# Kernel tuning notes

Measured on AMD Instinct MI355X. Metric: run time of the kernel, lower is better.

The kernel has to match this reference:

```python
import jax, jax.numpy as jnp
import numpy as np

M, B, T, D, P = 3, 128, 512, 1024, 256  # modalities, batch, time, d_model, projection_dim
LN_EPS = 1e-5
NORM_EPS = 1e-12


def setup_inputs() -> dict:
    key = jax.random.key(0)
    ks = jax.random.split(key, 7)
    s1 = 1.0 / np.sqrt(D)
    s2 = 1.0 / np.sqrt(D)
    return {
        "feats": jax.random.normal(ks[0], (M, B, T, D), dtype=jnp.float32),
        "W1": jax.random.uniform(ks[1], (M, D, D), jnp.float32, -s1, s1),
        "b1": jax.random.uniform(ks[2], (M, D), jnp.float32, -s1, s1),
        "W2": jax.random.uniform(ks[3], (M, D, P), jnp.float32, -s2, s2),
        "b2": jax.random.uniform(ks[4], (M, P), jnp.float32, -s2, s2),
        "gamma": jnp.ones((M, P), jnp.float32),
        "beta": jnp.zeros((M, P), jnp.float32),
    }


def reference(feats, W1, b1, W2, b2, gamma, beta):
    # Mean-pool over time: [M,B,T,D] -> [M,B,D]
    pooled = feats.mean(axis=2)
    # Linear(d_model, d_model) + exact GELU (dropout is identity at inference)
    h = jax.nn.gelu(jnp.einsum('mbd,mde->mbe', pooled, W1) + b1[:, None, :],
                    approximate=False)
    # Linear(d_model, projection_dim)
    z = jnp.einsum('mbd,mdp->mbp', h, W2) + b2[:, None, :]
    # LayerNorm over last dim
    mu = z.mean(axis=-1, keepdims=True)
    var = jnp.mean((z - mu) ** 2, axis=-1, keepdims=True)
    z = (z - mu) / jnp.sqrt(var + LN_EPS) * gamma[:, None, :] + beta[:, None, :]
    # F.normalize (cosine path): divide by max(l2_norm, eps)
    n = jnp.sqrt(jnp.sum(z * z, axis=-1, keepdims=True))
    return z / jnp.maximum(n, NORM_EPS)  # [M, B, P]
```

## Files before the change

kernel.cpp:

```cpp
#include <hip/hip_runtime.h>
#include <math.h>

#define M_ 3
#define B_ 128
#define T_ 512
#define D_ 1024
#define P_ 256
#define TC 4
#define BM1 32
#define BN1 64
#define BK1 64
#define LDA1 (BK1 + 4)
#define G  2

__global__ __launch_bounds__(256) void pool_partial(const float* __restrict__ feats,
                                                    float* __restrict__ partial) {
    int blk = blockIdx.x;
    int tc  = blk & (TC - 1);
    int mb  = blk / TC;
    int tid = threadIdx.x;
    const int TSTEP = T_ / TC;
    const float4* src = (const float4*)feats + ((size_t)mb * T_ + (size_t)tc * TSTEP) * (D_ / 4) + tid;
    float4 a0 = make_float4(0.f, 0.f, 0.f, 0.f);
    float4 a1 = a0, a2 = a0, a3 = a0;
    for (int t = 0; t < TSTEP; t += 4) {
        float4 v0 = src[0 * (D_ / 4)];
        float4 v1 = src[1 * (D_ / 4)];
        float4 v2 = src[2 * (D_ / 4)];
        float4 v3 = src[3 * (D_ / 4)];
        src += 4 * (D_ / 4);
        a0.x += v0.x; a0.y += v0.y; a0.z += v0.z; a0.w += v0.w;
        a1.x += v1.x; a1.y += v1.y; a1.z += v1.z; a1.w += v1.w;
        a2.x += v2.x; a2.y += v2.y; a2.z += v2.z; a2.w += v2.w;
        a3.x += v3.x; a3.y += v3.y; a3.z += v3.z; a3.w += v3.w;
    }
    float4 s;
    s.x = (a0.x + a1.x) + (a2.x + a3.x);
    s.y = (a0.y + a1.y) + (a2.y + a3.y);
    s.z = (a0.z + a1.z) + (a2.z + a3.z);
    s.w = (a0.w + a1.w) + (a2.w + a3.w);
    ((float4*)partial)[((size_t)mb * TC + tc) * (D_ / 4) + tid] = s;
}

__global__ __launch_bounds__(256) void pool_finalize(const float* __restrict__ partial,
                                                     float* __restrict__ pooled) {
    int idx = blockIdx.x * 256 + threadIdx.x;
    int mb  = idx >> 8;
    int d4  = idx & 255;
    const float4* p4 = (const float4*)partial;
    float4 s = make_float4(0.f, 0.f, 0.f, 0.f);
#pragma unroll
    for (int tc = 0; tc < TC; ++tc) {
        float4 v = p4[((size_t)mb * TC + tc) * (D_ / 4) + d4];
        s.x += v.x; s.y += v.y; s.z += v.z; s.w += v.w;
    }
    const float inv = 1.0f / (float)T_;
    s.x *= inv; s.y *= inv; s.z *= inv; s.w *= inv;
    ((float4*)pooled)[idx] = s;
}

__global__ __launch_bounds__(256) void gemm1_gelu(const float* __restrict__ pooled,
                                                  const float* __restrict__ W1,
                                                  const float* __restrict__ b1,
                                                  float* __restrict__ h) {
    __shared__ float As[BM1][LDA1];
    __shared__ float Bs[BK1][BN1];
    int m  = blockIdx.z;
    int b0 = blockIdx.y * BM1;
    int e0 = blockIdx.x * BN1;
    int tid = threadIdx.x;
    int ar  = tid >> 4;
    int ac4 = tid & 15;
    int ty  = tid >> 4;
    int tx  = tid & 15;

    const float* Abase = pooled + ((size_t)m * B_ + b0) * D_;
    const float* Bbase = W1 + (size_t)m * D_ * D_ + e0;

    float4 acc0 = make_float4(0.f, 0.f, 0.f, 0.f);
    float4 acc1 = make_float4(0.f, 0.f, 0.f, 0.f);

    for (int k0 = 0; k0 < D_; k0 += BK1) {
        float4 av0 = *(const float4*)(Abase + (size_t)ar * D_ + k0 + ac4 * 4);
        float4 av1 = *(const float4*)(Abase + (size_t)(ar + 16) * D_ + k0 + ac4 * 4);
        float4 bv0 = *(const float4*)(Bbase + (size_t)(k0 + ar) * D_ + ac4 * 4);
        float4 bv1 = *(const float4*)(Bbase + (size_t)(k0 + ar + 16) * D_ + ac4 * 4);
        float4 bv2 = *(const float4*)(Bbase + (size_t)(k0 + ar + 32) * D_ + ac4 * 4);
        float4 bv3 = *(const float4*)(Bbase + (size_t)(k0 + ar + 48) * D_ + ac4 * 4);
        __syncthreads();
        *(float4*)&As[ar][ac4 * 4]      = av0;
        *(float4*)&As[ar + 16][ac4 * 4] = av1;
        *(float4*)&Bs[ar][ac4 * 4]      = bv0;
        *(float4*)&Bs[ar + 16][ac4 * 4] = bv1;
        *(float4*)&Bs[ar + 32][ac4 * 4] = bv2;
        *(float4*)&Bs[ar + 48][ac4 * 4] = bv3;
        __syncthreads();
#pragma unroll
        for (int k = 0; k < BK1; ++k) {
            float a0 = As[2 * ty][k];
            float a1 = As[2 * ty + 1][k];
            float4 b = *(float4*)&Bs[k][tx * 4];
            acc0.x += a0 * b.x; acc0.y += a0 * b.y; acc0.z += a0 * b.z; acc0.w += a0 * b.w;
            acc1.x += a1 * b.x; acc1.y += a1 * b.y; acc1.z += a1 * b.z; acc1.w += a1 * b.w;
        }
    }
    int col = e0 + tx * 4;
    float4 bb = *(const float4*)(b1 + m * D_ + col);
    float4 z0, z1;
    z0.x = acc0.x + bb.x; z0.y = acc0.y + bb.y; z0.z = acc0.z + bb.z; z0.w = acc0.w + bb.w;
    z1.x = acc1.x + bb.x; z1.y = acc1.y + bb.y; z1.z = acc1.z + bb.z; z1.w = acc1.w + bb.w;
    const float is2 = 0.70710678118654752f;
    float4 g0, g1;
    g0.x = 0.5f * z0.x * (1.0f + erff(z0.x * is2));
    g0.y = 0.5f * z0.y * (1.0f + erff(z0.y * is2));
    g0.z = 0.5f * z0.z * (1.0f + erff(z0.z * is2));
    g0.w = 0.5f * z0.w * (1.0f + erff(z0.w * is2));
    g1.x = 0.5f * z1.x * (1.0f + erff(z1.x * is2));
    g1.y = 0.5f * z1.y * (1.0f + erff(z1.y * is2));
    g1.z = 0.5f * z1.z * (1.0f + erff(z1.z * is2));
    g1.w = 0.5f * z1.w * (1.0f + erff(z1.w * is2));
    int row0 = b0 + 2 * ty;
    *(float4*)&h[((size_t)m * B_ + row0) * D_ + col]     = g0;
    *(float4*)&h[((size_t)m * B_ + row0 + 1) * D_ + col] = g1;
}

__global__ __launch_bounds__(256) void gemm2_ln(const float* __restrict__ h,
                                                const float* __restrict__ W2,
                                                const float* __restrict__ b2,
                                                const float* __restrict__ gamma,
                                                const float* __restrict__ beta,
                                                float* __restrict__ out) {
    int m  = blockIdx.y;
    int b0 = blockIdx.x * G;
    int tid = threadIdx.x;
    int lane = tid & 63, w = tid >> 6;

    __shared__ float red1[4][G];
    __shared__ float red2[4][G];

    const float* W2base = W2 + (size_t)m * D_ * P_ + tid;
    const float* hbase  = h + ((size_t)m * B_ + b0) * D_;

    float acc[G];
#pragma unroll
    for (int g = 0; g < G; ++g) acc[g] = 0.f;

#pragma unroll 4
    for (int k4 = 0; k4 < D_ / 4; ++k4) {
        float w0 = W2base[(size_t)(4 * k4 + 0) * P_];
        float w1 = W2base[(size_t)(4 * k4 + 1) * P_];
        float w2 = W2base[(size_t)(4 * k4 + 2) * P_];
        float w3 = W2base[(size_t)(4 * k4 + 3) * P_];
#pragma unroll
        for (int g = 0; g < G; ++g) {
            float4 hv = *(const float4*)(hbase + (size_t)g * D_ + 4 * k4);
            acc[g] += hv.x * w0 + hv.y * w1 + hv.z * w2 + hv.w * w3;
        }
    }

    float bias = b2[m * P_ + tid];
    float gm   = gamma[m * P_ + tid];
    float bt   = beta[m * P_ + tid];

    float z[G];
#pragma unroll
    for (int g = 0; g < G; ++g) z[g] = acc[g] + bias;

#pragma unroll
    for (int g = 0; g < G; ++g) {
        float s1 = z[g], s2 = z[g] * z[g];
        for (int off = 32; off > 0; off >>= 1) {
            s1 += __shfl_xor(s1, off);
            s2 += __shfl_xor(s2, off);
        }
        if (lane == 0) { red1[w][g] = s1; red2[w][g] = s2; }
    }
    __syncthreads();
#pragma unroll
    for (int g = 0; g < G; ++g) {
        float s1 = (red1[0][g] + red1[1][g]) + (red1[2][g] + red1[3][g]);
        float s2 = (red2[0][g] + red2[1][g]) + (red2[2][g] + red2[3][g]);
        float mu  = s1 * (1.0f / P_);
        float var = s2 * (1.0f / P_) - mu * mu;
        float inv = 1.0f / sqrtf(var + 1e-5f);
        z[g] = (z[g] - mu) * inv * gm + bt;
    }
    __syncthreads();

#pragma unroll
    for (int g = 0; g < G; ++g) {
        float s = z[g] * z[g];
        for (int off = 32; off > 0; off >>= 1) s += __shfl_xor(s, off);
        if (lane == 0) red1[w][g] = s;
    }
    __syncthreads();
#pragma unroll
    for (int g = 0; g < G; ++g) {
        float s = (red1[0][g] + red1[1][g]) + (red1[2][g] + red1[3][g]);
        float n = sqrtf(s);
        out[((size_t)m * B_ + b0 + g) * P_ + tid] = z[g] / fmaxf(n, 1e-12f);
    }
}

extern "C" void kernel_launch(void* const* d_in, const int* in_sizes, int n_in,
                              void* d_out, int out_size, void* d_ws, size_t ws_size,
                              hipStream_t stream) {
    const float* feats = (const float*)d_in[0];
    const float* W1    = (const float*)d_in[1];
    const float* b1    = (const float*)d_in[2];
    const float* W2    = (const float*)d_in[3];
    const float* b2    = (const float*)d_in[4];
    const float* gamma = (const float*)d_in[5];
    const float* beta  = (const float*)d_in[6];
    float* out = (float*)d_out;

    float* wsf     = (float*)d_ws;
    float* partial = wsf;
    float* pooled  = wsf + (size_t)M_ * B_ * TC * D_;
    float* hbuf    = pooled + (size_t)M_ * B_ * D_;

    pool_partial<<<M_ * B_ * TC, 256, 0, stream>>>(feats, partial);
    pool_finalize<<<(M_ * B_ * D_ / 4) / 256, 256, 0, stream>>>(partial, pooled);
    dim3 g3(D_ / BN1, B_ / BM1, M_);
    gemm1_gelu<<<g3, 256, 0, stream>>>(pooled, W1, b1, hbuf);
    dim3 g4(B_ / G, M_);
    gemm2_ln<<<g4, 256, 0, stream>>>(hbuf, W2, b2, gamma, beta, out);
}
```

Before: 219.6 us.

## Fuse pool finalize into GEMM1, split-K both GEMMs, cast W2 to bf16

Removes the pool_finalize kernel by having GEMM1 sum the TC=2 partial sums and scale by 1/T while loading A. Pooling now uses two time chunks per row with eight accumulators instead of four. Both GEMMs run 512 threads with an intra-block split-K whose halves are combined through shared memory. Extra blocks in the pooling launch convert W2 to packed bf16 so GEMM2 reads half the weight bytes, at the cost of reduced precision in the second projection.

```diff
diff --git a/kernel.cpp b/kernel.cpp
--- a/kernel.cpp
+++ b/kernel.cpp
@@ -6,200 +6,221 @@
 #define T_ 512
 #define D_ 1024
 #define P_ 256
-#define TC 4
+#define TC 2
+#define NRIDER 64
 #define BM1 32
 #define BN1 64
-#define BK1 64
-#define LDA1 (BK1 + 4)
-#define G  2
-
-__global__ __launch_bounds__(256) void pool_partial(const float* __restrict__ feats,
-                                                    float* __restrict__ partial) {
+
+__device__ __forceinline__ unsigned int f2bf(float f) {
+    unsigned int x = __float_as_uint(f);
+    return (x + 0x7fffu + ((x >> 16) & 1u)) >> 16;
+}
+
+__global__ __launch_bounds__(256) void pool_and_cast(const float* __restrict__ feats,
+                                                     const float* __restrict__ W2,
+                                                     float* __restrict__ partial,
+                                                     unsigned int* __restrict__ w2p) {
     int blk = blockIdx.x;
-    int tc  = blk & (TC - 1);
-    int mb  = blk / TC;
     int tid = threadIdx.x;
+    if (blk < NRIDER) {
+        const int TOT = M_ * (D_ / 2) * P_;
+        for (int i = blk * 256 + tid; i < TOT; i += NRIDER * 256) {
+            int p  = i & (P_ - 1);
+            int k2 = (i >> 8) & (D_ / 2 - 1);
+            int m  = i >> 17;
+            size_t base = (size_t)m * D_ * P_ + (size_t)(2 * k2) * P_ + p;
+            float f0 = W2[base];
+            float f1 = W2[base + P_];
+            w2p[i] = f2bf(f0) | (f2bf(f1) << 16);
+        }
+        return;
+    }
+    blk -= NRIDER;
+    int tc = blk & (TC - 1);
+    int mb = blk / TC;
     const int TSTEP = T_ / TC;
     const float4* src = (const float4*)feats + ((size_t)mb * T_ + (size_t)tc * TSTEP) * (D_ / 4) + tid;
     float4 a0 = make_float4(0.f, 0.f, 0.f, 0.f);
-    float4 a1 = a0, a2 = a0, a3 = a0;
-    for (int t = 0; t < TSTEP; t += 4) {
+    float4 a1 = a0, a2 = a0, a3 = a0, a4 = a0, a5 = a0, a6 = a0, a7 = a0;
+    for (int t = 0; t < TSTEP; t += 8) {
         float4 v0 = src[0 * (D_ / 4)];
         float4 v1 = src[1 * (D_ / 4)];
         float4 v2 = src[2 * (D_ / 4)];
         float4 v3 = src[3 * (D_ / 4)];
-        src += 4 * (D_ / 4);
+        float4 v4 = src[4 * (D_ / 4)];
+        float4 v5 = src[5 * (D_ / 4)];
+        float4 v6 = src[6 * (D_ / 4)];
+        float4 v7 = src[7 * (D_ / 4)];
+        src += 8 * (D_ / 4);
         a0.x += v0.x; a0.y += v0.y; a0.z += v0.z; a0.w += v0.w;
         a1.x += v1.x; a1.y += v1.y; a1.z += v1.z; a1.w += v1.w;
         a2.x += v2.x; a2.y += v2.y; a2.z += v2.z; a2.w += v2.w;
         a3.x += v3.x; a3.y += v3.y; a3.z += v3.z; a3.w += v3.w;
+        a4.x += v4.x; a4.y += v4.y; a4.z += v4.z; a4.w += v4.w;
+        a5.x += v5.x; a5.y += v5.y; a5.z += v5.z; a5.w += v5.w;
+        a6.x += v6.x; a6.y += v6.y; a6.z += v6.z; a6.w += v6.w;
+        a7.x += v7.x; a7.y += v7.y; a7.z += v7.z; a7.w += v7.w;
     }
     float4 s;
-    s.x = (a0.x + a1.x) + (a2.x + a3.x);
-    s.y = (a0.y + a1.y) + (a2.y + a3.y);
-    s.z = (a0.z + a1.z) + (a2.z + a3.z);
-    s.w = (a0.w + a1.w) + (a2.w + a3.w);
+    s.x = ((a0.x + a1.x) + (a2.x + a3.x)) + ((a4.x + a5.x) + (a6.x + a7.x));
+    s.y = ((a0.y + a1.y) + (a2.y + a3.y)) + ((a4.y + a5.y) + (a6.y + a7.y));
+    s.z = ((a0.z + a1.z) + (a2.z + a3.z)) + ((a4.z + a5.z) + (a6.z + a7.z));
+    s.w = ((a0.w + a1.w) + (a2.w + a3.w)) + ((a4.w + a5.w) + (a6.w + a7.w));
     ((float4*)partial)[((size_t)mb * TC + tc) * (D_ / 4) + tid] = s;
 }
 
-__global__ __launch_bounds__(256) void pool_finalize(const float* __restrict__ partial,
-                                                     float* __restrict__ pooled) {
-    int idx = blockIdx.x * 256 + threadIdx.x;
-    int mb  = idx >> 8;
-    int d4  = idx & 255;
-    const float4* p4 = (const float4*)partial;
-    float4 s = make_float4(0.f, 0.f, 0.f, 0.f);
-#pragma unroll
-    for (int tc = 0; tc < TC; ++tc) {
-        float4 v = p4[((size_t)mb * TC + tc) * (D_ / 4) + d4];
-        s.x += v.x; s.y += v.y; s.z += v.z; s.w += v.w;
-    }
-    const float inv = 1.0f / (float)T_;
-    s.x *= inv; s.y *= inv; s.z *= inv; s.w *= inv;
-    ((float4*)pooled)[idx] = s;
-}
-
-__global__ __launch_bounds__(256) void gemm1_gelu(const float* __restrict__ pooled,
+__global__ __launch_bounds__(512) void gemm1_gelu(const float* __restrict__ partial,
                                                   const float* __restrict__ W1,
                                                   const float* __restrict__ b1,
                                                   float* __restrict__ h) {
-    __shared__ float As[BM1][LDA1];
-    __shared__ float Bs[BK1][BN1];
+    __shared__ float As[2][BM1][68];
+    __shared__ float Bs[2][64][68];
     int m  = blockIdx.z;
     int b0 = blockIdx.y * BM1;
     int e0 = blockIdx.x * BN1;
-    int tid = threadIdx.x;
-    int ar  = tid >> 4;
-    int ac4 = tid & 15;
-    int ty  = tid >> 4;
-    int tx  = tid & 15;
-
-    const float* Abase = pooled + ((size_t)m * B_ + b0) * D_;
-    const float* Bbase = W1 + (size_t)m * D_ * D_ + e0;
+    int tid  = threadIdx.x;
+    int half = tid >> 8;
+    int t    = tid & 255;
+    int ar  = t >> 4;
+    int ac4 = t & 15;
+    int ty  = t >> 4;
+    int tx  = t & 15;
+
+    const float* Ab = partial + (size_t)(m * B_ + b0) * TC * D_;
+    const float* Bb = W1 + (size_t)m * D_ * D_ + e0;
+    const float inv = 1.0f / (float)T_;
 
     float4 acc0 = make_float4(0.f, 0.f, 0.f, 0.f);
     float4 acc1 = make_float4(0.f, 0.f, 0.f, 0.f);
 
-    for (int k0 = 0; k0 < D_; k0 += BK1) {
-        float4 av0 = *(const float4*)(Abase + (size_t)ar * D_ + k0 + ac4 * 4);
-        float4 av1 = *(const float4*)(Abase + (size_t)(ar + 16) * D_ + k0 + ac4 * 4);
-        float4 bv0 = *(const float4*)(Bbase + (size_t)(k0 + ar) * D_ + ac4 * 4);
-        float4 bv1 = *(const float4*)(Bbase + (size_t)(k0 + ar + 16) * D_ + ac4 * 4);
-        float4 bv2 = *(const float4*)(Bbase + (size_t)(k0 + ar + 32) * D_ + ac4 * 4);
-        float4 bv3 = *(const float4*)(Bbase + (size_t)(k0 + ar + 48) * D_ + ac4 * 4);
+    for (int kk = 0; kk < 8; ++kk) {
+        int k0 = half * 512 + kk * 64;
+        const float* Ar0 = Ab + (size_t)(TC * ar) * D_ + k0 + 4 * ac4;
+        const float* Ar1 = Ab + (size_t)(TC * (ar + 16)) * D_ + k0 + 4 * ac4;
+        float4 p00 = *(const float4*)(Ar0);
+        float4 p01 = *(const float4*)(Ar0 + D_);
+        float4 p10 = *(const float4*)(Ar1);
+        float4 p11 = *(const float4*)(Ar1 + D_);
+        float4 bv0 = *(const float4*)(Bb + (size_t)(k0 + ar) * D_ + 4 * ac4);
+        float4 bv1 = *(const float4*)(Bb + (size_t)(k0 + ar + 16) * D_ + 4 * ac4);
+        float4 bv2 = *(const float4*)(Bb + (size_t)(k0 + ar + 32) * D_ + 4 * ac4);
+        float4 bv3 = *(const float4*)(Bb + (size_t)(k0 + ar + 48) * D_ + 4 * ac4);
         __syncthreads();
-        *(float4*)&As[ar][ac4 * 4]      = av0;
-        *(float4*)&As[ar + 16][ac4 * 4] = av1;
-        *(float4*)&Bs[ar][ac4 * 4]      = bv0;
-        *(float4*)&Bs[ar + 16][ac4 * 4] = bv1;
-        *(float4*)&Bs[ar + 32][ac4 * 4] = bv2;
-        *(float4*)&Bs[ar + 48][ac4 * 4] = bv3;
+        float4 av0, av1;
+        av0.x = (p00.x + p01.x) * inv; av0.y = (p00.y + p01.y) * inv;
+        av0.z = (p00.z + p01.z) * inv; av0.w = (p00.w + p01.w) * inv;
+        av1.x = (p10.x + p11.x) * inv; av1.y = (p10.y + p11.y) * inv;
+        av1.z = (p10.z + p11.z) * inv; av1.w = (p10.w + p11.w) * inv;
+        *(float4*)&As[half][ar][4 * ac4]      = av0;
+        *(float4*)&As[half][ar + 16][4 * ac4] = av1;
+        *(float4*)&Bs[half][ar][4 * ac4]      = bv0;
+        *(float4*)&Bs[half][ar + 16][4 * ac4] = bv1;
+        *(float4*)&Bs[half][ar + 32][4 * ac4] = bv2;
+        *(float4*)&Bs[half][ar + 48][4 * ac4] = bv3;
         __syncthreads();
 #pragma unroll
-        for (int k = 0; k < BK1; ++k) {
-            float a0 = As[2 * ty][k];
-            float a1 = As[2 * ty + 1][k];
-            float4 b = *(float4*)&Bs[k][tx * 4];
-            acc0.x += a0 * b.x; acc0.y += a0 * b.y; acc0.z += a0 * b.z; acc0.w += a0 * b.w;
-            acc1.x += a1 * b.x; acc1.y += a1 * b.y; acc1.z += a1 * b.z; acc1.w += a1 * b.w;
+        for (int k = 0; k < 64; ++k) {
+            float A0 = As[half][2 * ty][k];
+            float A1 = As[half][2 * ty + 1][k];
+            float4 bb = *(const float4*)&Bs[half][k][4 * tx];
+            acc0.x += A0 * bb.x; acc0.y += A0 * bb.y; acc0.z += A0 * bb.z; acc0.w += A0 * bb.w;
+            acc1.x += A1 * bb.x; acc1.y += A1 * bb.y; acc1.z += A1 * bb.z; acc1.w += A1 * bb.w;
         }
     }
-    int col = e0 + tx * 4;
-    float4 bb = *(const float4*)(b1 + m * D_ + col);
-    float4 z0, z1;
-    z0.x = acc0.x + bb.x; z0.y = acc0.y + bb.y; z0.z = acc0.z + bb.z; z0.w = acc0.w + bb.w;
-    z1.x = acc1.x + bb.x; z1.y = acc1.y + bb.y; z1.z = acc1.z + bb.z; z1.w = acc1.w + bb.w;
-    const float is2 = 0.70710678118654752f;
-    float4 g0, g1;
-    g0.x = 0.5f * z0.x * (1.0f + erff(z0.x * is2));
-    g0.y = 0.5f * z0.y * (1.0f + erff(z0.y * is2));
-    g0.z = 0.5f * z0.z * (1.0f + erff(z0.z * is2));
-    g0.w = 0.5f * z0.w * (1.0f + erff(z0.w * is2));
-    g1.x = 0.5f * z1.x * (1.0f + erff(z1.x * is2));
-    g1.y = 0.5f * z1.y * (1.0f + erff(z1.y * is2));
-    g1.z = 0.5f * z1.z * (1.0f + erff(z1.z * is2));
-    g1.w = 0.5f * z1.w * (1.0f + erff(z1.w * is2));
-    int row0 = b0 + 2 * ty;
-    *(float4*)&h[((size_t)m * B_ + row0) * D_ + col]     = g0;
-    *(float4*)&h[((size_t)m * B_ + row0 + 1) * D_ + col] = g1;
-}
-
-__global__ __launch_bounds__(256) void gemm2_ln(const float* __restrict__ h,
-                                                const float* __restrict__ W2,
+    __syncthreads();
+    float* zb = &As[0][0][0];
+    if (half == 0) {
+        *(float4*)&zb[(2 * ty) * 68 + 4 * tx]     = acc0;
+        *(float4*)&zb[(2 * ty + 1) * 68 + 4 * tx] = acc1;
+    }
+    __syncthreads();
+    if (half == 1) {
+        int col = e0 + 4 * tx;
+        float4 bb = *(const float4*)(b1 + m * D_ + col);
+        float4 z0 = *(const float4*)&zb[(2 * ty) * 68 + 4 * tx];
+        float4 z1 = *(const float4*)&zb[(2 * ty + 1) * 68 + 4 * tx];
+        z0.x += acc0.x + bb.x; z0.y += acc0.y + bb.y; z0.z += acc0.z + bb.z; z0.w += acc0.w + bb.w;
+        z1.x += acc1.x + bb.x; z1.y += acc1.y + bb.y; z1.z += acc1.z + bb.z; z1.w += acc1.w + bb.w;
+        const float is2 = 0.70710678118654752f;
+        float4 g0, g1;
+        g0.x = 0.5f * z0.x * (1.0f + erff(z0.x * is2));
+        g0.y = 0.5f * z0.y * (1.0f + erff(z0.y * is2));
+        g0.z = 0.5f * z0.z * (1.0f + erff(z0.z * is2));
+        g0.w = 0.5f * z0.w * (1.0f + erff(z0.w * is2));
+        g1.x = 0.5f * z1.x * (1.0f + erff(z1.x * is2));
+        g1.y = 0.5f * z1.y * (1.0f + erff(z1.y * is2));
+        g1.z = 0.5f * z1.z * (1.0f + erff(z1.z * is2));
+        g1.w = 0.5f * z1.w * (1.0f + erff(z1.w * is2));
+        int row0 = b0 + 2 * ty;
+        *(float4*)&h[((size_t)m * B_ + row0) * D_ + col]     = g0;
+        *(float4*)&h[((size_t)m * B_ + row0 + 1) * D_ + col] = g1;
+    }
+}
+
+__global__ __launch_bounds__(512) void gemm2_ln(const float* __restrict__ h,
+                                                const unsigned int* __restrict__ w2p,
                                                 const float* __restrict__ b2,
                                                 const float* __restrict__ gamma,
                                                 const float* __restrict__ beta,
                                                 float* __restrict__ out) {
     int m  = blockIdx.y;
-    int b0 = blockIdx.x * G;
-    int tid = threadIdx.x;
-    int lane = tid & 63, w = tid >> 6;
-
-    __shared__ float red1[4][G];
-    __shared__ float red2[4][G];
-
-    const float* W2base = W2 + (size_t)m * D_ * P_ + tid;
-    const float* hbase  = h + ((size_t)m * B_ + b0) * D_;
-
-    float acc[G];
-#pragma unroll
-    for (int g = 0; g < G; ++g) acc[g] = 0.f;
-
+    int b0 = blockIdx.x * 2;
+    int tid  = threadIdx.x;
+    int p    = tid & 255;
+    int half = tid >> 8;
+    int lane = tid & 63;
+    int w    = (tid >> 6) & 3;
+
+    __shared__ float accs[2][2][256];
+    __shared__ float redA[2][4];
+    __shared__ float redB[2][4];
+    __shared__ float redC[2][4];
+
+    const unsigned int* Wp = w2p + (size_t)m * (D_ / 2) * P_ + (size_t)half * 256 * P_ + p;
+    const float* hb = h + ((size_t)m * B_ + b0) * D_ + half * 512;
+
+    float acc0 = 0.f, acc1 = 0.f;
 #pragma unroll 4
-    for (int k4 = 0; k4 < D_ / 4; ++k4) {
-        float w0 = W2base[(size_t)(4 * k4 + 0) * P_];
-        float w1 = W2base[(size_t)(4 * k4 + 1) * P_];
-        float w2 = W2base[(size_t)(4 * k4 + 2) * P_];
-        float w3 = W2base[(size_t)(4 * k4 + 3) * P_];
-#pragma unroll
-        for (int g = 0; g < G; ++g) {
-            float4 hv = *(const float4*)(hbase + (size_t)g * D_ + 4 * k4);
-            acc[g] += hv.x * w0 + hv.y * w1 + hv.z * w2 + hv.w * w3;
-        }
-    }
-
-    float bias = b2[m * P_ + tid];
-    float gm   = gamma[m * P_ + tid];
-    float bt   = beta[m * P_ + tid];
-
-    float z[G];
-#pragma unroll
-    for (int g = 0; g < G; ++g) z[g] = acc[g] + bias;
-
-#pragma unroll
-    for (int g = 0; g < G; ++g) {
-        float s1 = z[g], s2 = z[g] * z[g];
-        for (int off = 32; off > 0; off >>= 1) {
-            s1 += __shfl_xor(s1, off);
-            s2 += __shfl_xor(s2, off);
-        }
-        if (lane == 0) { red1[w][g] = s1; red2[w][g] = s2; }
-    }
-    __syncthreads();
-#pragma unroll
-    for (int g = 0; g < G; ++g) {
-        float s1 = (red1[0][g] + red1[1][g]) + (red1[2][g] + red1[3][g]);
-        float s2 = (red2[0][g] + red2[1][g]) + (red2[2][g] + red2[3][g]);
-        float mu  = s1 * (1.0f / P_);
-        float var = s2 * (1.0f / P_) - mu * mu;
-        float inv = 1.0f / sqrtf(var + 1e-5f);
-        z[g] = (z[g] - mu) * inv * gm + bt;
-    }
-    __syncthreads();
-
-#pragma unroll
-    for (int g = 0; g < G; ++g) {
-        float s = z[g] * z[g];
-        for (int off = 32; off > 0; off >>= 1) s += __shfl_xor(s, off);
-        if (lane == 0) red1[w][g] = s;
-    }
-    __syncthreads();
-#pragma unroll
-    for (int g = 0; g < G; ++g) {
-        float s = (red1[0][g] + red1[1][g]) + (red1[2][g] + red1[3][g]);
-        float n = sqrtf(s);
-        out[((size_t)m * B_ + b0 + g) * P_ + tid] = z[g] / fmaxf(n, 1e-12f);
-    }
+    for (int q = 0; q < 128; ++q) {
+        unsigned int u0 = Wp[(size_t)(2 * q) * P_];
+        unsigned int u1 = Wp[(size_t)(2 * q + 1) * P_];
+        float w0 = __uint_as_float(u0 << 16);
+        float w1 = __uint_as_float(u0 & 0xffff0000u);
+        float w2 = __uint_as_float(u1 << 16);
+        float w3 = __uint_as_float(u1 & 0xffff0000u);
+        float4 h0 = *(const float4*)(hb + 4 * q);
+        float4 h1 = *(const float4*)(hb + D_ + 4 * q);
+        acc0 += h0.x * w0 + h0.y * w1 + h0.z * w2 + h0.w * w3;
+        acc1 += h1.x * w0 + h1.y * w1 + h1.z * w2 + h1.w * w3;
+    }
+    accs[half][0][p] = acc0;
+    accs[half][1][p] = acc1;
+    __syncthreads();
+
+    int g = half;
+    float z = accs[0][g][p] + accs[1][g][p] + b2[m * P_ + p];
+
+    float s1 = z, s2 = z * z;
+    for (int off = 32; off > 0; off >>= 1) {
+        s1 += __shfl_xor(s1, off);
+        s2 += __shfl_xor(s2, off);
+    }
+    if (lane == 0) { redA[g][w] = s1; redB[g][w] = s2; }
+    __syncthreads();
+    s1 = (redA[g][0] + redA[g][1]) + (redA[g][2] + redA[g][3]);
+    s2 = (redB[g][0] + redB[g][1]) + (redB[g][2] + redB[g][3]);
+    float mu  = s1 * (1.0f / P_);
+    float var = s2 * (1.0f / P_) - mu * mu;
+    float inv = 1.0f / sqrtf(var + 1e-5f);
+    z = (z - mu) * inv * gamma[m * P_ + p] + beta[m * P_ + p];
+
+    float s = z * z;
+    for (int off = 32; off > 0; off >>= 1) s += __shfl_xor(s, off);
+    if (lane == 0) redC[g][w] = s;
+    __syncthreads();
+    s = (redC[g][0] + redC[g][1]) + (redC[g][2] + redC[g][3]);
+    float n = sqrtf(s);
+    out[((size_t)m * B_ + b0 + g) * P_ + p] = z / fmaxf(n, 1e-12f);
 }
 
 extern "C" void kernel_launch(void* const* d_in, const int* in_sizes, int n_in,
@@ -214,15 +235,14 @@
     const float* beta  = (const float*)d_in[6];
     float* out = (float*)d_out;
 
-    float* wsf     = (float*)d_ws;
-    float* partial = wsf;
-    float* pooled  = wsf + (size_t)M_ * B_ * TC * D_;
-    float* hbuf    = pooled + (size_t)M_ * B_ * D_;
-
-    pool_partial<<<M_ * B_ * TC, 256, 0, stream>>>(feats, partial);
-    pool_finalize<<<(M_ * B_ * D_ / 4) / 256, 256, 0, stream>>>(partial, pooled);
-    dim3 g3(D_ / BN1, B_ / BM1, M_);
-    gemm1_gelu<<<g3, 256, 0, stream>>>(pooled, W1, b1, hbuf);
-    dim3 g4(B_ / G, M_);
-    gemm2_ln<<<g4, 256, 0, stream>>>(hbuf, W2, b2, gamma, beta, out);
-}
+    float* wsf = (float*)d_ws;
+    float*        partial = wsf;
+    unsigned int* w2p     = (unsigned int*)(wsf + 786432);
+    float*        hbuf    = wsf + 786432 + 393216;
+
+    pool_and_cast<<<NRIDER + M_ * B_ * TC, 256, 0, stream>>>(feats, W2, partial, w2p);
+    dim3 g2(D_ / BN1, B_ / BM1, M_);
+    gemm1_gelu<<<g2, 512, 0, stream>>>(partial, W1, b1, hbuf);
+    dim3 g3(B_ / 2, M_);
+    gemm2_ln<<<g3, 512, 0, stream>>>(hbuf, w2p, b2, gamma, beta, out);
+}
```

Result: faster. 190.5 us (-13.2%).
